# Performance work log

Measured on AMD Instinct MI355X. Metric: run time of the kernel, lower is better.

Reference implementation:

```python
import jax, jax.numpy as jnp
import numpy as np
import math

B, T, C = 2, 2048, 2048
H, KV, HD = 16, 4, 128  # num_heads, num_kv_heads, head_dim
REP = H // KV


def _rope_tables(T, hd, base=10000.0):
    inv_freq = 1.0 / (base ** (np.arange(0, hd, 2, dtype=np.float32) / hd))  # [hd/2]
    t = np.arange(T, dtype=np.float32)
    freqs = np.outer(t, inv_freq)                 # [T, hd/2]
    emb = np.concatenate([freqs, freqs], axis=-1)  # [T, hd]
    return jnp.asarray(np.cos(emb)), jnp.asarray(np.sin(emb))


def setup_inputs() -> dict:
    key = jax.random.key(0)
    ks = jax.random.split(key, 5)
    cos, sin = _rope_tables(T, HD)
    std = 0.02
    return {
        "x": jax.random.normal(ks[0], (B, T, C), dtype=jnp.float32),
        "cos": cos,
        "sin": sin,
        "Wq": jax.random.normal(ks[1], (C, H * HD), dtype=jnp.float32) * std,
        "Wk": jax.random.normal(ks[2], (C, KV * HD), dtype=jnp.float32) * std,
        "Wv": jax.random.normal(ks[3], (C, KV * HD), dtype=jnp.float32) * std,
        "Wo": jax.random.normal(ks[4], (H * HD, C), dtype=jnp.float32) * std,
    }


def _rotate_half(t):
    h = t.shape[-1] // 2
    return jnp.concatenate([-t[..., h:], t[..., :h]], axis=-1)


def reference(x, cos, sin, Wq, Wk, Wv, Wo):
    Bx, Tx, Cx = x.shape
    q = (x @ Wq).reshape(Bx, Tx, H, HD).transpose(0, 2, 1, 3)   # [B,H,T,hd]
    k = (x @ Wk).reshape(Bx, Tx, KV, HD).transpose(0, 2, 1, 3)  # [B,KV,T,hd]
    v = (x @ Wv).reshape(Bx, Tx, KV, HD).transpose(0, 2, 1, 3)
    c = cos[None, None]  # [1,1,T,hd]
    s = sin[None, None]
    q = q * c + _rotate_half(q) * s
    k = k * c + _rotate_half(k) * s
    # repeat_kv: expand KV heads to H heads (interleave within groups)
    k = jnp.repeat(k, REP, axis=1)  # [B,H,T,hd]
    v = jnp.repeat(v, REP, axis=1)
    scores = jnp.einsum("bhqd,bhkd->bhqk", q, k) / math.sqrt(HD)
    causal = jnp.triu(jnp.full((Tx, Tx), float("-inf"), dtype=scores.dtype), k=1)
    scores = jax.nn.softmax(scores + causal[None, None], axis=-1)
    out = jnp.einsum("bhqk,bhkd->bhqd", scores, v)  # [B,H,T,hd]
    out = out.transpose(0, 2, 1, 3).reshape(Bx, Tx, H * HD)
    return out @ Wo
```

## Files before the change

kernel.cpp:

```cpp
#include <hip/hip_runtime.h>
#include <hip/hip_bf16.h>
#include <math.h>

typedef __bf16 bf16_t;
typedef __bf16 bf16x8 __attribute__((ext_vector_type(8)));
typedef float f32x4 __attribute__((ext_vector_type(4)));

constexpr int Bc = 2, Tc = 2048, Cdim = 2048, Hc = 16, KVc = 4, HDc = 128;
constexpr int Mc = Bc * Tc;
constexpr int Nqkv = 3072;

typedef const __attribute__((address_space(1))) void* as1_cptr;
typedef __attribute__((address_space(3))) void* as3_ptr;

__device__ __forceinline__ void gload_lds16(const bf16_t* g, bf16_t* l) {
  __builtin_amdgcn_global_load_lds((as1_cptr)(const void*)g, (as3_ptr)(void*)l, 16, 0, 0);
}

__global__ void k_cvt_bf16(const float* __restrict__ in, bf16_t* __restrict__ out) {
  int i = (blockIdx.x * 256 + threadIdx.x) * 8;
  float4 a = *(const float4*)(in + i);
  float4 b = *(const float4*)(in + i + 4);
  bf16x8 v;
  v[0] = (bf16_t)a.x; v[1] = (bf16_t)a.y; v[2] = (bf16_t)a.z; v[3] = (bf16_t)a.w;
  v[4] = (bf16_t)b.x; v[5] = (bf16_t)b.y; v[6] = (bf16_t)b.z; v[7] = (bf16_t)b.w;
  *(bf16x8*)(out + i) = v;
}

__global__ void k_w_trans(const float* __restrict__ W, bf16_t* __restrict__ Wt,
                          int K, int N) {
  __shared__ alignas(16) bf16_t tile[64][72];
  const int k0 = blockIdx.x * 64, n0 = blockIdx.y * 64;
  const int t = threadIdx.x;
#pragma unroll
  for (int i = 0; i < 4; ++i) {
    int idx = t + i * 256;
    int r = idx >> 4;
    int c4 = (idx & 15) * 4;
    float4 v = *(const float4*)(W + (size_t)(k0 + r) * N + n0 + c4);
    tile[r][c4 + 0] = (bf16_t)v.x; tile[r][c4 + 1] = (bf16_t)v.y;
    tile[r][c4 + 2] = (bf16_t)v.z; tile[r][c4 + 3] = (bf16_t)v.w;
  }
  __syncthreads();
#pragma unroll
  for (int i = 0; i < 4; ++i) {
    int idx = t + i * 256;
    int n = idx >> 4;
    int kc = (idx & 15) * 4;
    alignas(8) bf16_t o[4];
#pragma unroll
    for (int j = 0; j < 4; ++j) o[j] = tile[kc + j][n];
    *(uint2*)(Wt + (size_t)(n0 + n) * K + k0 + kc) = *(uint2*)o;
  }
}

template <typename OutT>
__global__ __launch_bounds__(256, 2) void k_gemm_bt(
    const bf16_t* __restrict__ A, const bf16_t* __restrict__ Bt,
    OutT* __restrict__ Cout, int M, int N, int K) {
  __shared__ alignas(16) bf16_t Ash[128 * 64];
  __shared__ alignas(16) bf16_t Bsh[128 * 64];
  const int tid = threadIdx.x;
  const int wave = tid >> 6, lane = tid & 63;
  const int col = lane & 15, quad = lane >> 4;
  const int m0 = blockIdx.y * 128, n0 = blockIdx.x * 128;
  const int wr = wave >> 1, wc = wave & 1;

  f32x4 acc[4][4];
#pragma unroll
  for (int i = 0; i < 4; ++i)
#pragma unroll
    for (int j = 0; j < 4; ++j) acc[i][j] = f32x4{0.f, 0.f, 0.f, 0.f};

  const int lrow = lane >> 3;
  const int lkc8 = (lane & 7) ^ lrow;

  for (int k0 = 0; k0 < K; k0 += 64) {
    __syncthreads();
#pragma unroll
    for (int i = 0; i < 4; ++i) {
      const int rb = wave * 32 + i * 8;
      gload_lds16(A + (size_t)(m0 + rb + lrow) * K + k0 + lkc8 * 8, Ash + rb * 64);
      gload_lds16(Bt + (size_t)(n0 + rb + lrow) * K + k0 + lkc8 * 8, Bsh + rb * 64);
    }
    __syncthreads();
#pragma unroll
    for (int kc = 0; kc < 2; ++kc) {
      bf16x8 af[4], bfr[4];
#pragma unroll
      for (int mt = 0; mt < 4; ++mt) {
        const int m = wr * 64 + mt * 16 + col;
        const int slot = (kc * 4 + quad) ^ (m & 7);
        af[mt] = *(const bf16x8*)(Ash + m * 64 + slot * 8);
      }
#pragma unroll
      for (int nt = 0; nt < 4; ++nt) {
        const int n = wc * 64 + nt * 16 + col;
        const int slot = (kc * 4 + quad) ^ (n & 7);
        bfr[nt] = *(const bf16x8*)(Bsh + n * 64 + slot * 8);
      }
#pragma unroll
      for (int mt = 0; mt < 4; ++mt)
#pragma unroll
        for (int nt = 0; nt < 4; ++nt)
          acc[mt][nt] = __builtin_amdgcn_mfma_f32_16x16x32_bf16(
              af[mt], bfr[nt], acc[mt][nt], 0, 0, 0);
    }
  }
#pragma unroll
  for (int mt = 0; mt < 4; ++mt)
#pragma unroll
    for (int i = 0; i < 4; ++i) {
      const int row = m0 + wr * 64 + mt * 16 + quad * 4 + i;
#pragma unroll
      for (int nt = 0; nt < 4; ++nt)
        Cout[(size_t)row * N + n0 + wc * 64 + nt * 16 + col] = (OutT)acc[mt][nt][i];
    }
}

__global__ void k_rope2(const bf16_t* __restrict__ in, const float* __restrict__ cs,
                        const float* __restrict__ sn, bf16_t* __restrict__ outQ,
                        bf16_t* __restrict__ outK) {
  const int idx = blockIdx.x * 256 + threadIdx.x;
  const int d = idx & 63;
  const int hh = (idx >> 6) % 20;
  const int bt = idx / (64 * 20);
  const int t = bt & (Tc - 1);
  const int b = bt >> 11;
  const bool isQ = hh < 16;
  const int h = isQ ? hh : hh - 16;
  const int colb = isQ ? h * HDc : 2048 + h * HDc;
  const size_t bi = (size_t)(b * Tc + t) * Nqkv + colb;
  const float x0 = (float)in[bi + d];
  const float x1 = (float)in[bi + d + 64];
  const float c0 = cs[t * HDc + d], c1 = cs[t * HDc + d + 64];
  const float s0 = sn[t * HDc + d], s1 = sn[t * HDc + d + 64];
  bf16_t* op = isQ ? outQ + ((size_t)(b * Hc + h) * Tc + t) * HDc
                   : outK + ((size_t)(b * KVc + h) * Tc + t) * HDc;
  op[d]      = (bf16_t)(x0 * c0 - x1 * s0);
  op[d + 64] = (bf16_t)(x1 * c1 + x0 * s1);
}

__global__ void k_vtrans(const bf16_t* __restrict__ v, bf16_t* __restrict__ vt,
                         int in_stride, int col_off) {
  __shared__ alignas(16) bf16_t tile[64][136];
  const int t0 = blockIdx.x * 64;
  const int kv = blockIdx.y, b = blockIdx.z;
  const int tid = threadIdx.x;
#pragma unroll
  for (int i = 0; i < 4; ++i) {
    int idx = tid + i * 256;
    int r = idx >> 4;
    int ch = idx & 15;
    const bf16_t* gp = v + (size_t)(b * Tc + t0 + r) * in_stride + col_off + kv * HDc + ch * 8;
    *(uint4*)&tile[r][ch * 8] = *(const uint4*)gp;
  }
  __syncthreads();
#pragma unroll
  for (int i = 0; i < 4; ++i) {
    int idx = tid + i * 256;
    int d = idx >> 3;
    int tc = idx & 7;
    alignas(16) bf16_t o[8];
#pragma unroll
    for (int j = 0; j < 8; ++j) o[j] = tile[tc * 8 + j][d];
    bf16_t* gp = vt + ((size_t)(b * KVc + kv) * HDc + d) * Tc + t0 + tc * 8;
    *(uint4*)gp = *(uint4*)o;
  }
}

__global__ __launch_bounds__(256, 2) void k_attn(
    const bf16_t* __restrict__ Qp, const bf16_t* __restrict__ Kp,
    const bf16_t* __restrict__ Vt, bf16_t* __restrict__ Oout) {
  constexpr float sc2 = 0.08838834764831845f * 1.4426950408889634f;
  __shared__ alignas(16) bf16_t Ksh[2][64 * 128];
  __shared__ alignas(16) bf16_t Vsh[2][128 * 64];
  __shared__ alignas(16) bf16_t Psh[4][16 * 64];

  const int i2 = blockIdx.x, h = blockIdx.y, b = blockIdx.z;
  const int kvh = h >> 2;
  const int tid = threadIdx.x, wave = tid >> 6, lane = tid & 63;
  const int col = lane & 15, quad = lane >> 4;

  const bf16_t* Kb = Kp + (size_t)(b * KVc + kvh) * Tc * HDc;
  const bf16_t* Vb = Vt + (size_t)(b * KVc + kvh) * HDc * Tc;
  const bf16_t* Qbh = Qp + (size_t)(b * Hc + h) * Tc * HDc;

  const int st_kr = lane >> 4, st_kc8 = lane & 15;
  const int st_vr = lane >> 3, st_vc8 = lane & 7;

  const int qb0 = 31 - i2, qb1 = i2;
  const int n0it = qb0 + 1;
  const int ntot = qb0 + qb1 + 2;

  int q0 = qb0 * 64 + wave * 16;

  bf16x8 qf[4];
  {
    const bf16_t* qbase = Qbh + (size_t)(q0 + col) * HDc;
#pragma unroll
    for (int kc = 0; kc < 4; ++kc) {
      bf16x8 raw = *(const bf16x8*)(qbase + kc * 32 + quad * 8);
#pragma unroll
      for (int e = 0; e < 8; ++e) qf[kc][e] = (bf16_t)((float)raw[e] * sc2);
    }
  }

  f32x4 o_acc[8];
#pragma unroll
  for (int nb = 0; nb < 8; ++nb) o_acc[nb] = f32x4{0.f, 0.f, 0.f, 0.f};
  float l_i[4] = {0.f, 0.f, 0.f, 0.f};

#pragma unroll
  for (int i = 0; i < 4; ++i) {
    const int rb = wave * 16 + i * 4;
    const int r = rb + st_kr;
    const int kc8 = st_kc8 ^ (r & 7);
    gload_lds16(Kb + (size_t)r * HDc + kc8 * 8, &Ksh[0][rb * 128]);
    const int db = wave * 32 + i * 8;
    const int d = db + st_vr;
    const int tc8 = st_vc8 ^ (d & 7);
    gload_lds16(Vb + (size_t)d * Tc + tc8 * 8, &Vsh[0][db * 64]);
  }

#pragma unroll 1
  for (int j = 0; j < ntot; ++j) {
    const int cur = j & 1;
    const bool diag = (j == qb0) || (j == ntot - 1);
    asm volatile("s_barrier" ::: "memory");
    {
      const int jn = (j + 1 < ntot) ? (j + 1) : (ntot - 1);
      const int tn = (jn < n0it) ? jn : (jn - n0it);
      const int kbn = tn * 64;
#pragma unroll
      for (int i = 0; i < 4; ++i) {
        const int rb = wave * 16 + i * 4;
        const int r = rb + st_kr;
        const int kc8 = st_kc8 ^ (r & 7);
        gload_lds16(Kb + (size_t)(kbn + r) * HDc + kc8 * 8, &Ksh[cur ^ 1][rb * 128]);
        const int db = wave * 32 + i * 8;
        const int d = db + st_vr;
        const int tc8 = st_vc8 ^ (d & 7);
        gload_lds16(Vb + (size_t)d * Tc + kbn + tc8 * 8, &Vsh[cur ^ 1][db * 64]);
      }
    }
    asm volatile("s_waitcnt vmcnt(8)" ::: "memory");
    asm volatile("s_barrier" ::: "memory");

    const bf16_t* Kc = &Ksh[cur][0];
    const bf16_t* Vc = &Vsh[cur][0];

    f32x4 st[4];
#pragma unroll
    for (int tb = 0; tb < 4; ++tb) st[tb] = f32x4{0.f, 0.f, 0.f, 0.f};
#pragma unroll
    for (int kc = 0; kc < 4; ++kc)
#pragma unroll
      for (int tb = 0; tb < 4; ++tb) {
        const int r = tb * 16 + col;
        const int slot = (kc * 4 + quad) ^ (r & 7);
        bf16x8 kf = *(const bf16x8*)(Kc + r * 128 + slot * 8);
        st[tb] = __builtin_amdgcn_mfma_f32_16x16x32_bf16(qf[kc], kf, st[tb], 0, 0, 0);
      }

    bf16_t* pw = &Psh[wave][0];
    const int rowthr = wave * 16 + quad * 4;
#pragma unroll
    for (int i = 0; i < 4; ++i) {
      float e0 = exp2f(st[0][i]), e1 = exp2f(st[1][i]);
      float e2 = exp2f(st[2][i]), e3 = exp2f(st[3][i]);
      if (diag) {
        const int thr = rowthr + i;
        if (col      > thr) e0 = 0.f;
        if (16 + col > thr) e1 = 0.f;
        if (32 + col > thr) e2 = 0.f;
        if (48 + col > thr) e3 = 0.f;
      }
      l_i[i] += (e0 + e1) + (e2 + e3);
      const int r7 = (quad * 4 + i) & 7;
      const int rbase = (quad * 4 + i) * 64;
      const int c7 = col & 7, ch = col >> 3;
      pw[rbase + ((ch    ) ^ r7) * 8 + c7] = (bf16_t)e0;
      pw[rbase + ((ch + 2) ^ r7) * 8 + c7] = (bf16_t)e1;
      pw[rbase + ((ch + 4) ^ r7) * 8 + c7] = (bf16_t)e2;
      pw[rbase + ((ch + 6) ^ r7) * 8 + c7] = (bf16_t)e3;
    }
    asm volatile("s_waitcnt lgkmcnt(0)" ::: "memory");

#pragma unroll
    for (int kc = 0; kc < 2; ++kc) {
      const int slot = ((kc * 4) + quad) ^ (col & 7);
      const bf16x8 pf = *(const bf16x8*)(pw + col * 64 + slot * 8);
#pragma unroll
      for (int nb = 0; nb < 8; ++nb) {
        const int d = nb * 16 + col;
        const int vslot = (kc * 4 + quad) ^ (d & 7);
        bf16x8 vf = *(const bf16x8*)(Vc + d * 64 + vslot * 8);
        o_acc[nb] = __builtin_amdgcn_mfma_f32_16x16x32_bf16(pf, vf, o_acc[nb], 0, 0, 0);
      }
    }

    if (j == qb0) {
#pragma unroll
      for (int i = 0; i < 4; ++i) {
        float rs = l_i[i];
        rs += __shfl_xor(rs, 1);
        rs += __shfl_xor(rs, 2);
        rs += __shfl_xor(rs, 4);
        rs += __shfl_xor(rs, 8);
        const float inv = 1.0f / rs;
        const int qrow = q0 + quad * 4 + i;
        bf16_t* op = Oout + ((size_t)(b * Tc) + qrow) * (Hc * HDc) + h * HDc;
#pragma unroll
        for (int nb = 0; nb < 8; ++nb) op[nb * 16 + col] = (bf16_t)(o_acc[nb][i] * inv);
        l_i[i] = 0.f;
      }
#pragma unroll
      for (int nb = 0; nb < 8; ++nb) o_acc[nb] = f32x4{0.f, 0.f, 0.f, 0.f};
      q0 = qb1 * 64 + wave * 16;
      const bf16_t* qbase = Qbh + (size_t)(q0 + col) * HDc;
#pragma unroll
      for (int kc = 0; kc < 4; ++kc) {
        bf16x8 raw = *(const bf16x8*)(qbase + kc * 32 + quad * 8);
#pragma unroll
        for (int e = 0; e < 8; ++e) qf[kc][e] = (bf16_t)((float)raw[e] * sc2);
      }
    }
  }

#pragma unroll
  for (int i = 0; i < 4; ++i) {
    float rs = l_i[i];
    rs += __shfl_xor(rs, 1);
    rs += __shfl_xor(rs, 2);
    rs += __shfl_xor(rs, 4);
    rs += __shfl_xor(rs, 8);
    const float inv = 1.0f / rs;
    const int qrow = q0 + quad * 4 + i;
    bf16_t* op = Oout + ((size_t)(b * Tc) + qrow) * (Hc * HDc) + h * HDc;
#pragma unroll
    for (int nb = 0; nb < 8; ++nb) op[nb * 16 + col] = (bf16_t)(o_acc[nb][i] * inv);
  }
}

extern "C" void kernel_launch(void* const* d_in, const int* in_sizes, int n_in,
                              void* d_out, int out_size, void* d_ws, size_t ws_size,
                              hipStream_t stream) {
  (void)in_sizes; (void)n_in; (void)out_size; (void)ws_size;
  const float* x    = (const float*)d_in[0];
  const float* cosT = (const float*)d_in[1];
  const float* sinT = (const float*)d_in[2];
  const float* Wq   = (const float*)d_in[3];
  const float* Wk   = (const float*)d_in[4];
  const float* Wv   = (const float*)d_in[5];
  const float* Wo   = (const float*)d_in[6];
  float* out = (float*)d_out;

  char* ws = (char*)d_ws;
  size_t off = 0;
  auto take = [&](size_t bytes) { char* p = ws + off; off += (bytes + 255) & ~(size_t)255; return p; };

  bf16_t* xb    = (bf16_t*)take((size_t)Mc * Cdim * 2);
  bf16_t* Wqkvt = (bf16_t*)take((size_t)Nqkv * Cdim * 2);
  bf16_t* Wot   = (bf16_t*)take((size_t)Cdim * (Hc * HDc) * 2);
  bf16_t* qkv   = (bf16_t*)take((size_t)Mc * Nqkv * 2);
  bf16_t* Kp    = (bf16_t*)take((size_t)Mc * (KVc * HDc) * 2);
  bf16_t* Vt    = (bf16_t*)take((size_t)Mc * (KVc * HDc) * 2);
  bf16_t* Wqt = Wqkvt;
  bf16_t* Wkt = Wqkvt + (size_t)2048 * Cdim;
  bf16_t* Wvt = Wqkvt + (size_t)2560 * Cdim;
  bf16_t* Qp   = xb;
  bf16_t* attn = qkv;

  k_cvt_bf16<<<dim3((Mc * Cdim) / 2048), dim3(256), 0, stream>>>(x, xb);
  k_w_trans<<<dim3(Cdim / 64, 2048 / 64), dim3(256), 0, stream>>>(Wq, Wqt, Cdim, 2048);
  k_w_trans<<<dim3(Cdim / 64, 512 / 64), dim3(256), 0, stream>>>(Wk, Wkt, Cdim, 512);
  k_w_trans<<<dim3(Cdim / 64, 512 / 64), dim3(256), 0, stream>>>(Wv, Wvt, Cdim, 512);
  k_w_trans<<<dim3((Hc * HDc) / 64, Cdim / 64), dim3(256), 0, stream>>>(Wo, Wot, Hc * HDc, Cdim);
  k_gemm_bt<bf16_t><<<dim3(Nqkv / 128, Mc / 128), dim3(256), 0, stream>>>(
      xb, Wqkvt, qkv, Mc, Nqkv, Cdim);
  k_rope2<<<dim3((Bc * Tc * 20 * 64) / 256), dim3(256), 0, stream>>>(
      qkv, cosT, sinT, Qp, Kp);
  k_vtrans<<<dim3(Tc / 64, KVc, Bc), dim3(256), 0, stream>>>(qkv, Vt, Nqkv, 2560);
  k_attn<<<dim3(16, Hc, Bc), dim3(256), 0, stream>>>(Qp, Kp, Vt, attn);
  k_gemm_bt<float><<<dim3(Cdim / 128, Mc / 128), dim3(256), 0, stream>>>(
      attn, Wot, out, Mc, Cdim, Hc * HDc);
}
```

Before: 309.9 us.

## Compute transposed scores and feed P to PV MFMA via permlane swaps instead of LDS

```diff
diff --git a/kernel.cpp b/kernel.cpp
--- a/kernel.cpp
+++ b/kernel.cpp
@@ -15,6 +15,18 @@
 
 __device__ __forceinline__ void gload_lds16(const bf16_t* g, bf16_t* l) {
   __builtin_amdgcn_global_load_lds((as1_cptr)(const void*)g, (as3_ptr)(void*)l, 16, 0, 0);
+}
+
+__device__ __forceinline__ unsigned int cvt_pk_bf16(float lo, float hi) {
+  unsigned int r;
+  asm("v_cvt_pk_bf16_f32 %0, %1, %2" : "=v"(r) : "v"(lo), "v"(hi));
+  return r;
+}
+__device__ __forceinline__ void perm32swap(unsigned int& a, unsigned int& b) {
+  asm("v_permlane32_swap_b32 %0, %1" : "+v"(a), "+v"(b));
+}
+__device__ __forceinline__ void perm16swap(unsigned int& a, unsigned int& b) {
+  asm("v_permlane16_swap_b32 %0, %1" : "+v"(a), "+v"(b));
 }
 
 __global__ void k_cvt_bf16(const float* __restrict__ in, bf16_t* __restrict__ out) {
@@ -175,7 +187,6 @@
   constexpr float sc2 = 0.08838834764831845f * 1.4426950408889634f;
   __shared__ alignas(16) bf16_t Ksh[2][64 * 128];
   __shared__ alignas(16) bf16_t Vsh[2][128 * 64];
-  __shared__ alignas(16) bf16_t Psh[4][16 * 64];
 
   const int i2 = blockIdx.x, h = blockIdx.y, b = blockIdx.z;
   const int kvh = h >> 2;
@@ -194,6 +205,7 @@
   const int ntot = qb0 + qb1 + 2;
 
   int q0 = qb0 * 64 + wave * 16;
+  const int qr = wave * 16 + col;
 
   bf16x8 qf[4];
   {
@@ -209,7 +221,7 @@
   f32x4 o_acc[8];
 #pragma unroll
   for (int nb = 0; nb < 8; ++nb) o_acc[nb] = f32x4{0.f, 0.f, 0.f, 0.f};
-  float l_i[4] = {0.f, 0.f, 0.f, 0.f};
+  float l_i = 0.f;
 
 #pragma unroll
   for (int i = 0; i < 4; ++i) {
@@ -260,37 +272,37 @@
         const int r = tb * 16 + col;
         const int slot = (kc * 4 + quad) ^ (r & 7);
         bf16x8 kf = *(const bf16x8*)(Kc + r * 128 + slot * 8);
-        st[tb] = __builtin_amdgcn_mfma_f32_16x16x32_bf16(qf[kc], kf, st[tb], 0, 0, 0);
-      }
-
-    bf16_t* pw = &Psh[wave][0];
-    const int rowthr = wave * 16 + quad * 4;
-#pragma unroll
-    for (int i = 0; i < 4; ++i) {
-      float e0 = exp2f(st[0][i]), e1 = exp2f(st[1][i]);
-      float e2 = exp2f(st[2][i]), e3 = exp2f(st[3][i]);
+        st[tb] = __builtin_amdgcn_mfma_f32_16x16x32_bf16(kf, qf[kc], st[tb], 0, 0, 0);
+      }
+
+    unsigned int pwrd[4][2];
+#pragma unroll
+    for (int tb = 0; tb < 4; ++tb) {
+      const int kvb = tb * 16 + quad * 4;
+      float e0 = exp2f(st[tb][0]), e1 = exp2f(st[tb][1]);
+      float e2 = exp2f(st[tb][2]), e3 = exp2f(st[tb][3]);
       if (diag) {
-        const int thr = rowthr + i;
-        if (col      > thr) e0 = 0.f;
-        if (16 + col > thr) e1 = 0.f;
-        if (32 + col > thr) e2 = 0.f;
-        if (48 + col > thr) e3 = 0.f;
-      }
-      l_i[i] += (e0 + e1) + (e2 + e3);
-      const int r7 = (quad * 4 + i) & 7;
-      const int rbase = (quad * 4 + i) * 64;
-      const int c7 = col & 7, ch = col >> 3;
-      pw[rbase + ((ch    ) ^ r7) * 8 + c7] = (bf16_t)e0;
-      pw[rbase + ((ch + 2) ^ r7) * 8 + c7] = (bf16_t)e1;
-      pw[rbase + ((ch + 4) ^ r7) * 8 + c7] = (bf16_t)e2;
-      pw[rbase + ((ch + 6) ^ r7) * 8 + c7] = (bf16_t)e3;
-    }
-    asm volatile("s_waitcnt lgkmcnt(0)" ::: "memory");
+        e0 = (kvb + 0 > qr) ? 0.f : e0;
+        e1 = (kvb + 1 > qr) ? 0.f : e1;
+        e2 = (kvb + 2 > qr) ? 0.f : e2;
+        e3 = (kvb + 3 > qr) ? 0.f : e3;
+      }
+      l_i += (e0 + e1) + (e2 + e3);
+      pwrd[tb][0] = cvt_pk_bf16(e0, e1);
+      pwrd[tb][1] = cvt_pk_bf16(e2, e3);
+    }
 
 #pragma unroll
     for (int kc = 0; kc < 2; ++kc) {
-      const int slot = ((kc * 4) + quad) ^ (col & 7);
-      const bf16x8 pf = *(const bf16x8*)(pw + col * 64 + slot * 8);
+      unsigned int a0 = pwrd[2 * kc][0], b0 = pwrd[2 * kc + 1][0];
+      unsigned int a1 = pwrd[2 * kc][1], b1 = pwrd[2 * kc + 1][1];
+      perm32swap(a0, b0);
+      perm32swap(a1, b1);
+      perm16swap(a0, b0);
+      perm16swap(a1, b1);
+      union { unsigned int w[4]; bf16x8 v; } u;
+      u.w[0] = a0; u.w[1] = a1; u.w[2] = b0; u.w[3] = b1;
+      const bf16x8 pf = u.v;
 #pragma unroll
       for (int nb = 0; nb < 8; ++nb) {
         const int d = nb * 16 + col;
@@ -301,20 +313,19 @@
     }
 
     if (j == qb0) {
+      float rs = l_i;
+      rs += __shfl_xor(rs, 16);
+      rs += __shfl_xor(rs, 32);
+      const float inv = 1.0f / rs;
 #pragma unroll
       for (int i = 0; i < 4; ++i) {
-        float rs = l_i[i];
-        rs += __shfl_xor(rs, 1);
-        rs += __shfl_xor(rs, 2);
-        rs += __shfl_xor(rs, 4);
-        rs += __shfl_xor(rs, 8);
-        const float inv = 1.0f / rs;
+        const float iq = __shfl(inv, quad * 4 + i);
         const int qrow = q0 + quad * 4 + i;
         bf16_t* op = Oout + ((size_t)(b * Tc) + qrow) * (Hc * HDc) + h * HDc;
 #pragma unroll
-        for (int nb = 0; nb < 8; ++nb) op[nb * 16 + col] = (bf16_t)(o_acc[nb][i] * inv);
-        l_i[i] = 0.f;
-      }
+        for (int nb = 0; nb < 8; ++nb) op[nb * 16 + col] = (bf16_t)(o_acc[nb][i] * iq);
+      }
+      l_i = 0.f;
 #pragma unroll
       for (int nb = 0; nb < 8; ++nb) o_acc[nb] = f32x4{0.f, 0.f, 0.f, 0.f};
       q0 = qb1 * 64 + wave * 16;
@@ -328,18 +339,19 @@
     }
   }
 
-#pragma unroll
-  for (int i = 0; i < 4; ++i) {
-    float rs = l_i[i];
-    rs += __shfl_xor(rs, 1);
-    rs += __shfl_xor(rs, 2);
-    rs += __shfl_xor(rs, 4);
-    rs += __shfl_xor(rs, 8);
+  {
+    float rs = l_i;
+    rs += __shfl_xor(rs, 16);
+    rs += __shfl_xor(rs, 32);
     const float inv = 1.0f / rs;
-    const int qrow = q0 + quad * 4 + i;
-    bf16_t* op = Oout + ((size_t)(b * Tc) + qrow) * (Hc * HDc) + h * HDc;
-#pragma unroll
-    for (int nb = 0; nb < 8; ++nb) op[nb * 16 + col] = (bf16_t)(o_acc[nb][i] * inv);
+#pragma unroll
+    for (int i = 0; i < 4; ++i) {
+      const float iq = __shfl(inv, quad * 4 + i);
+      const int qrow = q0 + quad * 4 + i;
+      bf16_t* op = Oout + ((size_t)(b * Tc) + qrow) * (Hc * HDc) + h * HDc;
+#pragma unroll
+      for (int nb = 0; nb < 8; ++nb) op[nb * 16 + col] = (bf16_t)(o_acc[nb][i] * iq);
+    }
   }
 }
 
```

Result: no change. 306.7 us (-1.0%).
